# Optimization experiments

Hardware: AMD Instinct MI355X
Metric: run time of the kernel (lower is better)

The kernel has to match this reference:

```python
import jax, jax.numpy as jnp
import numpy as np
import math

T_LEN, BATCH, DIN, DH, DT = 512, 64, 512, 512, 128


def _u(key, shape, std):
    return jax.random.uniform(key, shape, jnp.float32, -std, std)


def setup_inputs() -> dict:
    key = jax.random.key(0)
    ks = jax.random.split(key, 32)
    std = 1.0 / math.sqrt(DH)
    inp = {
        'x': jax.random.normal(ks[0], (T_LEN, BATCH, DIN), jnp.float32),
        'topic': jax.random.normal(ks[1], (BATCH, DT), jnp.float32),
        'mask': jnp.ones((T_LEN, BATCH), jnp.float32),
        # weights stored as [in, out] (transpose of nn.Linear), uniform(-std, std)
        'W_x2zr': _u(ks[2], (DIN, 2 * DH), std),
        'W_tp2zr_x': _u(ks[3], (DT, 2 * DH), std),
        'W_xtp2z': _u(ks[4], (DH, DH), std),
        'b_xtp2z': _u(ks[5], (DH,), std),
        'W_xtp2r': _u(ks[6], (DH, DH), std),
        'b_xtp2r': _u(ks[7], (DH,), std),
        'W_h2zr': _u(ks[8], (DH, 2 * DH), std),
        'W_tp2zr_h': _u(ks[9], (DT, 2 * DH), std),
        'W_htp2z': _u(ks[10], (DH, DH), std),
        'W_htp2r': _u(ks[11], (DH, DH), std),
        'W_x2h': _u(ks[12], (DIN, DH), std),
        'W_tp2h_x': _u(ks[13], (DT, DH), std),
        'W_xtp2h': _u(ks[14], (DH, DH), std),
        'b_xtp2h': _u(ks[15], (DH,), std),
        'W_h2h': _u(ks[16], (DH, DH), std),
        'W_tp2h_h': _u(ks[17], (DT, DH), std),
        'W_htp2h': _u(ks[18], (DH, DH), std),
    }
    return inp


def _tpgru_forward(x, topic, mask,
                   W_x2zr, W_tp2zr_x, W_xtp2z, b_xtp2z, W_xtp2r, b_xtp2r,
                   W_h2zr, W_tp2zr_h, W_htp2z, W_htp2r,
                   W_x2h, W_tp2h_x, W_xtp2h, b_xtp2h,
                   W_h2h, W_tp2h_h, W_htp2h):
    # Precompute all time-parallel (input-side) projections outside the scan.
    ZR_x = x @ W_x2zr                          # [T,B,2H]
    tp_zr_x = topic @ W_tp2zr_x                # [B,2H]
    tp_zr_h = topic @ W_tp2zr_h                # [B,2H]
    Z_xtp, R_xtp = jnp.split(ZR_x * tp_zr_x[None], 2, axis=-1)
    ZR_xtp = jnp.concatenate([Z_xtp @ W_xtp2z + b_xtp2z,
                              R_xtp @ W_xtp2r + b_xtp2r], axis=-1)  # [T,B,2H]
    tp_h_x = topic @ W_tp2h_x                  # [B,H]
    tp_h_h = topic @ W_tp2h_h                  # [B,H]
    H_xtp = ((x @ W_x2h) * tp_h_x[None]) @ W_xtp2h + b_xtp2h        # [T,B,H]

    def step(h_, inputs):
        zr_xtp, h_xtp, m = inputs              # [B,2H], [B,H], [B]
        zr_htp = (h_ @ W_h2zr) * tp_zr_h
        z_htp, r_htp = jnp.split(zr_htp, 2, axis=-1)
        pre_zr = jax.nn.sigmoid(zr_xtp + jnp.concatenate(
            [z_htp @ W_htp2z, r_htp @ W_htp2r], axis=-1))
        z, r = jnp.split(pre_zr, 2, axis=-1)
        h = jnp.tanh(h_xtp + r * (((h_ @ W_h2h) * tp_h_h) @ W_htp2h))
        h = (1.0 - z) * h + z * h_
        m = m[:, None]
        h = m * h + (1.0 - m) * h_
        return h, h

    h0 = jnp.zeros((x.shape[1], W_h2h.shape[0]), x.dtype)
    hT, output = jax.lax.scan(step, h0, (ZR_xtp, H_xtp, mask))
    return output, hT[None]                    # [T,B,H], [1,B,H]


def reference(x, topic, mask,
              W_x2zr, W_tp2zr_x, W_xtp2z, b_xtp2z, W_xtp2r, b_xtp2r,
              W_h2zr, W_tp2zr_h, W_htp2z, W_htp2r,
              W_x2h, W_tp2h_x, W_xtp2h, b_xtp2h,
              W_h2h, W_tp2h_h, W_htp2h):
    return _tpgru_forward(x, topic, mask,
                          W_x2zr, W_tp2zr_x, W_xtp2z, b_xtp2z, W_xtp2r, b_xtp2r,
                          W_h2zr, W_tp2zr_h, W_htp2z, W_htp2r,
                          W_x2h, W_tp2h_x, W_xtp2h, b_xtp2h,
                          W_h2h, W_tp2h_h, W_htp2h)
```

## Files before the change

### kernel.cpp

```cpp
#include <hip/hip_runtime.h>
#include <stdint.h>
#include <stddef.h>


#define T_LEN 512
#define BATCH 64
#define DIN   512
#define DH    512
#define DT    128

typedef __attribute__((ext_vector_type(8))) short short8;
typedef __attribute__((ext_vector_type(4))) float f32x4;

static __device__ __forceinline__ float bf2f(unsigned short u) {
  unsigned v = ((unsigned)u) << 16;
  return __builtin_bit_cast(float, v);
}
static __device__ __forceinline__ unsigned short f2bf(float f) {
  unsigned v = __builtin_bit_cast(unsigned, f);
  unsigned r = (v + 0x7fffu + ((v >> 16) & 1u)) >> 16;
  return (unsigned short)r;
}
static __device__ __forceinline__ float sigmoid_f(float x) {
  return 1.f / (1.f + __expf(-x));
}
static __device__ __forceinline__ float tanh_f(float x) {
  float e = __expf(-2.f * fabsf(x));
  float t = (1.f - e) / (1.f + e);
  return copysignf(t, x);
}

static __device__ __forceinline__ void bstore_u16(unsigned short* p, unsigned short v) {
  __hip_atomic_store(p, v, __ATOMIC_RELAXED, __HIP_MEMORY_SCOPE_AGENT);
}

template<bool F32>
static __device__ __forceinline__ void load8(const void* p, size_t off, unsigned short* d) {
  if (F32) {
    const float4* q = (const float4*)((const float*)p + off);
    float4 a = q[0], b = q[1];
    d[0] = f2bf(a.x); d[1] = f2bf(a.y); d[2] = f2bf(a.z); d[3] = f2bf(a.w);
    d[4] = f2bf(b.x); d[5] = f2bf(b.y); d[6] = f2bf(b.z); d[7] = f2bf(b.w);
  } else {
    *(uint4*)d = *(const uint4*)((const unsigned short*)p + off);
  }
}

__global__ __launch_bounds__(256) void k_topic(
    const float* __restrict__ topic,
    const float* __restrict__ Wzx,
    const float* __restrict__ Wzh,
    const float* __restrict__ Whx,
    const float* __restrict__ Whh,
    float* __restrict__ tzx, float* __restrict__ tzh,
    float* __restrict__ thx, float* __restrict__ thh)
{
  const int b = blockIdx.x;
  __shared__ float tp[DT];
  if (threadIdx.x < DT) tp[threadIdx.x] = topic[b * DT + threadIdx.x];
  __syncthreads();
  for (int c = threadIdx.x; c < 3072; c += 256) {
    const float* wp; float* op; int ld, cc;
    if (c < 1024)      { wp = Wzx; ld = 1024; cc = c;        op = &tzx[b*1024 + cc]; }
    else if (c < 2048) { wp = Wzh; ld = 1024; cc = c - 1024; op = &tzh[b*1024 + cc]; }
    else if (c < 2560) { wp = Whx; ld = 512;  cc = c - 2048; op = &thx[b*512  + cc]; }
    else               { wp = Whh; ld = 512;  cc = c - 2560; op = &thh[b*512  + cc]; }
    float acc = 0.f;
    #pragma unroll 4
    for (int k = 0; k < DT; ++k) acc += tp[k] * wp[(size_t)k * ld + cc];
    *op = acc;
  }
}

template<int EPI, bool AF32, bool BF32>
__global__ __launch_bounds__(256) void gemm64(
    const void* __restrict__ A, int lda,
    const void* __restrict__ B1, int ldb1,
    const float* __restrict__ rs1, int ldrs1,
    const float* __restrict__ bias,
    unsigned short* __restrict__ C, int ldc, int K)
{
  __shared__ unsigned short As[64][48];
  __shared__ unsigned short Bs[64][48];
  const int tid = threadIdx.x;
  const int n0 = blockIdx.x * 64;
  const int m0 = blockIdx.y * 64;
  const int wv = tid >> 6, lane = tid & 63;
  const int lh = lane & 15, q8 = (lane >> 4) * 8;
  const int arow = tid >> 2, acol = (tid & 3) * 8;
  const int brow = tid >> 3, bcol = (tid & 7) * 8;
  f32x4 acc[4] = {{0,0,0,0},{0,0,0,0},{0,0,0,0},{0,0,0,0}};

  for (int k0 = 0; k0 < K; k0 += 32) {
    unsigned short av[8], bv[8];
    load8<AF32>(A, (size_t)(m0 + arow) * lda + (k0 + acol), av);
    load8<BF32>(B1, (size_t)(k0 + brow) * ldb1 + (n0 + bcol), bv);
    __syncthreads();
    *(uint4*)(&As[arow][acol]) = *(const uint4*)av;
    #pragma unroll
    for (int i = 0; i < 8; ++i) Bs[bcol + i][brow] = bv[i];
    __syncthreads();
    short8 af = *(const short8*)(&As[wv * 16 + lh][q8]);
    #pragma unroll
    for (int nt = 0; nt < 4; ++nt) {
      short8 bf = *(const short8*)(&Bs[nt * 16 + lh][q8]);
      acc[nt] = __builtin_amdgcn_mfma_f32_16x16x32_bf16(af, bf, acc[nt], 0, 0, 0);
    }
  }

  #pragma unroll
  for (int nt = 0; nt < 4; ++nt) {
    #pragma unroll
    for (int r = 0; r < 4; ++r) {
      int row = m0 + wv * 16 + (lane >> 4) * 4 + r;
      int colc = nt * 16 + lh;
      float v = acc[nt][r];
      if (EPI == 0) v *= rs1[(size_t)(row & 63) * ldrs1 + (n0 + colc)];
      else          v += bias[n0 + colc];
      C[(size_t)row * ldc + (n0 + colc)] = f2bf(v);
    }
  }
}

__global__ __launch_bounds__(256) void k_comb(
    const float* __restrict__ W1, int ld1, int off1,
    const float* __restrict__ W2,
    const float* __restrict__ S, int ldS, int offS,
    unsigned short* __restrict__ Cout)
{
  __shared__ unsigned short As[64][48];
  __shared__ unsigned short Bs[64][48];
  const int tid = threadIdx.x;
  const int n0 = blockIdx.x * 64;
  const int m0 = blockIdx.y * 64;
  const int b  = blockIdx.z;
  const int wv = tid >> 6, lane = tid & 63;
  const int lh = lane & 15, q8 = (lane >> 4) * 8;
  const int arow = tid >> 2, acol = (tid & 3) * 8;
  const int brow = tid >> 3, bcol = (tid & 7) * 8;
  const float* sv = S + (size_t)b * ldS + offS;
  f32x4 acc[4] = {{0,0,0,0},{0,0,0,0},{0,0,0,0},{0,0,0,0}};

  for (int k0 = 0; k0 < 512; k0 += 32) {
    unsigned short av[8], bv[8];
    {
      const float* p = W1 + (size_t)(m0 + arow) * ld1 + off1 + k0 + acol;
      float4 a = ((const float4*)p)[0], c2 = ((const float4*)p)[1];
      av[0]=f2bf(a.x); av[1]=f2bf(a.y); av[2]=f2bf(a.z); av[3]=f2bf(a.w);
      av[4]=f2bf(c2.x); av[5]=f2bf(c2.y); av[6]=f2bf(c2.z); av[7]=f2bf(c2.w);
    }
    {
      float sk = sv[k0 + brow];
      const float* p = W2 + (size_t)(k0 + brow) * 512 + n0 + bcol;
      float4 a = ((const float4*)p)[0], c2 = ((const float4*)p)[1];
      bv[0]=f2bf(a.x*sk); bv[1]=f2bf(a.y*sk); bv[2]=f2bf(a.z*sk); bv[3]=f2bf(a.w*sk);
      bv[4]=f2bf(c2.x*sk); bv[5]=f2bf(c2.y*sk); bv[6]=f2bf(c2.z*sk); bv[7]=f2bf(c2.w*sk);
    }
    __syncthreads();
    *(uint4*)(&As[arow][acol]) = *(const uint4*)av;
    #pragma unroll
    for (int i = 0; i < 8; ++i) Bs[bcol + i][brow] = bv[i];
    __syncthreads();
    short8 af = *(const short8*)(&As[wv * 16 + lh][q8]);
    #pragma unroll
    for (int nt = 0; nt < 4; ++nt) {
      short8 bf = *(const short8*)(&Bs[nt * 16 + lh][q8]);
      acc[nt] = __builtin_amdgcn_mfma_f32_16x16x32_bf16(af, bf, acc[nt], 0, 0, 0);
    }
  }

  #pragma unroll
  for (int nt = 0; nt < 4; ++nt) {
    #pragma unroll
    for (int r = 0; r < 4; ++r) {
      int row = m0 + wv * 16 + (lane >> 4) * 4 + r;
      int col = n0 + nt * 16 + lh;
      Cout[(size_t)b * 262144 + (size_t)row * 512 + col] = f2bf(acc[nt][r]);
    }
  }
}

static __device__ __forceinline__ void gbar(int* bar, int target) {
  asm volatile("s_waitcnt vmcnt(0)" ::: "memory");
  __syncthreads();
  if (threadIdx.x == 0) {
    __hip_atomic_fetch_add(bar, 1, __ATOMIC_RELAXED, __HIP_MEMORY_SCOPE_AGENT);
    while (__hip_atomic_load(bar, __ATOMIC_RELAXED, __HIP_MEMORY_SCOPE_AGENT) < target)
      __builtin_amdgcn_s_sleep(1);
  }
  __syncthreads();
}

static __device__ __forceinline__ void accum8(float* a, float hk, uint4 v) {
  unsigned u0 = v.x, u1 = v.y, u2 = v.z, u3 = v.w;
  a[0] += hk * __builtin_bit_cast(float, u0 << 16);
  a[1] += hk * __builtin_bit_cast(float, u0 & 0xffff0000u);
  a[2] += hk * __builtin_bit_cast(float, u1 << 16);
  a[3] += hk * __builtin_bit_cast(float, u1 & 0xffff0000u);
  a[4] += hk * __builtin_bit_cast(float, u2 << 16);
  a[5] += hk * __builtin_bit_cast(float, u2 & 0xffff0000u);
  a[6] += hk * __builtin_bit_cast(float, u3 << 16);
  a[7] += hk * __builtin_bit_cast(float, u3 & 0xffff0000u);
}

__global__ __launch_bounds__(512) void k_scan2(
    const unsigned short* __restrict__ Az,
    const unsigned short* __restrict__ Ar,
    const unsigned short* __restrict__ Ah,
    const unsigned short* __restrict__ ZRx,
    const unsigned short* __restrict__ Hx,
    const float* __restrict__ mask,
    unsigned short* hbuf,
    float* out, int* bar)
{
  const int g = blockIdx.x;
  const int b = g >> 3;
  const int o = g & 7;
  const int c0 = o * 64;
  const int t = threadIdx.x;
  const int chunk = t & 7;
  const int ph = t >> 3;
  __shared__ float hs[512];
  __shared__ float part[64][8][25];
  int* mybar = bar + b * 32;

  const size_t mbase = (size_t)b * 262144 + (size_t)ph * 512 + c0 + chunk * 8;
  const unsigned short* pz0 = Az + mbase;
  const unsigned short* pr0 = Ar + mbase;
  const unsigned short* pv0 = Ah + mbase;

  float hold = 0.f;
  int ep = 0;

  for (int tm = 0; tm < T_LEN; ++tm) {
    const int cur = tm & 1;
    const size_t itb = (size_t)tm * BATCH + b;
    float g_zx = 0.f, g_rx = 0.f, g_hx = 0.f, g_m = 0.f;
    if (t < 64) {
      int gc = c0 + t;
      g_zx = bf2f(ZRx[itb * 1024 + gc]);
      g_rx = bf2f(ZRx[itb * 1024 + 512 + gc]);
      g_hx = bf2f(Hx[itb * 512 + gc]);
      g_m  = mask[itb];
    }
    if (t < 256) {
      unsigned v = __hip_atomic_load(
          (const unsigned*)(hbuf + ((size_t)cur * 64 + b) * 512) + t,
          __ATOMIC_RELAXED, __HIP_MEMORY_SCOPE_AGENT);
      hs[2 * t]     = bf2f((unsigned short)(v & 0xffffu));
      hs[2 * t + 1] = bf2f((unsigned short)(v >> 16));
    }
    __syncthreads();

    float az[8] = {0,0,0,0,0,0,0,0};
    float ar[8] = {0,0,0,0,0,0,0,0};
    float av[8] = {0,0,0,0,0,0,0,0};
    #pragma unroll
    for (int j = 0; j < 8; ++j) {
      float hk = hs[ph + 64 * j];
      uint4 vz = *(const uint4*)(pz0 + (size_t)j * 64 * 512);
      uint4 vr = *(const uint4*)(pr0 + (size_t)j * 64 * 512);
      uint4 vv = *(const uint4*)(pv0 + (size_t)j * 64 * 512);
      accum8(az, hk, vz);
      accum8(ar, hk, vr);
      accum8(av, hk, vv);
    }
    #pragma unroll
    for (int e = 0; e < 8; ++e) {
      part[ph][chunk][e]      = az[e];
      part[ph][chunk][8 + e]  = ar[e];
      part[ph][chunk][16 + e] = av[e];
    }
    __syncthreads();

    if (t < 64) {
      int gc = c0 + t;
      int ch = t >> 3, e = t & 7;
      float sz = 0.f, sr = 0.f, sh = 0.f;
      #pragma unroll 8
      for (int p = 0; p < 64; ++p) {
        sz += part[p][ch][e];
        sr += part[p][ch][8 + e];
        sh += part[p][ch][16 + e];
      }
      float z  = sigmoid_f(sz + g_zx);
      float r  = sigmoid_f(sr + g_rx);
      float hv = tanh_f(g_hx + r * sh);
      float hnew = (1.f - z) * hv + z * hold;
      hnew = g_m * hnew + (1.f - g_m) * hold;
      hold = hnew;
      out[itb * 512 + gc] = hnew;
      if (tm == T_LEN - 1)
        out[(size_t)T_LEN * BATCH * 512 + (size_t)b * 512 + gc] = hnew;
      bstore_u16(hbuf + ((size_t)(cur ^ 1) * 64 + b) * 512 + gc, f2bf(hnew));
    }
    ++ep;
    gbar(mybar, 8 * ep);
  }
}

extern "C" void kernel_launch(void* const* d_in, const int* in_sizes, int n_in,
                              void* d_out, int out_size, void* d_ws, size_t ws_size,
                              hipStream_t stream) {
  (void)in_sizes; (void)n_in; (void)out_size; (void)ws_size;
  const float* x        = (const float*)d_in[0];
  const float* topic    = (const float*)d_in[1];
  const float* mask     = (const float*)d_in[2];
  const float* W_x2zr   = (const float*)d_in[3];
  const float* W_tp2zrx = (const float*)d_in[4];
  const float* W_xtp2z  = (const float*)d_in[5];
  const float* b_xtp2z  = (const float*)d_in[6];
  const float* W_xtp2r  = (const float*)d_in[7];
  const float* b_xtp2r  = (const float*)d_in[8];
  const float* W_h2zr   = (const float*)d_in[9];
  const float* W_tp2zrh = (const float*)d_in[10];
  const float* W_htp2z  = (const float*)d_in[11];
  const float* W_htp2r  = (const float*)d_in[12];
  const float* W_x2h    = (const float*)d_in[13];
  const float* W_tp2hx  = (const float*)d_in[14];
  const float* W_xtp2h  = (const float*)d_in[15];
  const float* b_xtp2h  = (const float*)d_in[16];
  const float* W_h2h    = (const float*)d_in[17];
  const float* W_tp2hh  = (const float*)d_in[18];
  const float* W_htp2h  = (const float*)d_in[19];
  float* out = (float*)d_out;

  char* w = (char*)d_ws;
  int*            bar  = (int*)w;            w += 8192;
  unsigned short* hbuf = (unsigned short*)w; w += (size_t)2 * BATCH * 512 * 2;
  float* tzx = (float*)w;           w += (size_t)BATCH * 1024 * 4;
  float* tzh = (float*)w;           w += (size_t)BATCH * 1024 * 4;
  float* thx = (float*)w;           w += (size_t)BATCH * 512 * 4;
  float* thh = (float*)w;           w += (size_t)BATCH * 512 * 4;
  unsigned short* ZRxtp = (unsigned short*)w; w += (size_t)T_LEN * BATCH * 1024 * 2;
  unsigned short* Hxtp  = (unsigned short*)w; w += (size_t)T_LEN * BATCH * 512 * 2;
  unsigned short* SCR   = (unsigned short*)w; w += (size_t)T_LEN * BATCH * 1024 * 2;
  unsigned short* AhM   = (unsigned short*)w; w += (size_t)BATCH * 512 * 512 * 2;
  unsigned short* ZRs = SCR;
  unsigned short* Xhs = SCR;
  unsigned short* AzM = SCR;
  unsigned short* ArM = SCR + (size_t)BATCH * 512 * 512;

  const int M = T_LEN * BATCH;

  hipMemsetAsync(bar, 0, 8192 + (size_t)2 * BATCH * 512 * 2, stream);

  k_topic<<<BATCH, 256, 0, stream>>>(topic, W_tp2zrx, W_tp2zrh, W_tp2hx, W_tp2hh,
                                     tzx, tzh, thx, thh);
  gemm64<0, true, true><<<dim3(1024/64, M/64), 256, 0, stream>>>(
      x, DIN, W_x2zr, 1024, tzx, 1024, nullptr, ZRs, 1024, DIN);
  gemm64<1, false, true><<<dim3(512/64, M/64), 256, 0, stream>>>(
      ZRs, 1024, W_xtp2z, 512, nullptr, 0, b_xtp2z, ZRxtp, 1024, 512);
  gemm64<1, false, true><<<dim3(512/64, M/64), 256, 0, stream>>>(
      ZRs + 512, 1024, W_xtp2r, 512, nullptr, 0, b_xtp2r, ZRxtp + 512, 1024, 512);
  gemm64<0, true, true><<<dim3(512/64, M/64), 256, 0, stream>>>(
      x, DIN, W_x2h, 512, thx, 512, nullptr, Xhs, 512, DIN);
  gemm64<1, false, true><<<dim3(512/64, M/64), 256, 0, stream>>>(
      Xhs, 512, W_xtp2h, 512, nullptr, 0, b_xtp2h, Hxtp, 512, 512);

  k_comb<<<dim3(8, 8, 64), 256, 0, stream>>>(W_h2zr, 1024,   0, W_htp2z, tzh, 1024,   0, AzM);
  k_comb<<<dim3(8, 8, 64), 256, 0, stream>>>(W_h2zr, 1024, 512, W_htp2r, tzh, 1024, 512, ArM);
  k_comb<<<dim3(8, 8, 64), 256, 0, stream>>>(W_h2h,   512,   0, W_htp2h, thh,  512,   0, AhM);

  k_scan2<<<512, 512, 0, stream>>>(AzM, ArM, AhM, ZRxtp, Hxtp, mask,
                                   hbuf, out, bar);
}
```

Before: 4.975 ms.

## Replace per-step atomic barrier with per-slice flag publishing in GRU scan

Drops the counter barrier (fetch-add plus spin) that every block hit each timestep. Each block now writes its packed bf16 hidden slice next to a per-slice step tag in a double-buffered publish area, and consumers spin on the eight tags before reading h. The final reduction is also split across 192 threads instead of 64. Each step should wait less, but correctness now rests on relaxed atomics plus the vmcnt wait ordering the data stores before the tag store.

```diff
diff --git a/kernel.cpp b/kernel.cpp
--- a/kernel.cpp
+++ b/kernel.cpp
@@ -28,10 +28,6 @@
   float e = __expf(-2.f * fabsf(x));
   float t = (1.f - e) / (1.f + e);
   return copysignf(t, x);
-}
-
-static __device__ __forceinline__ void bstore_u16(unsigned short* p, unsigned short v) {
-  __hip_atomic_store(p, v, __ATOMIC_RELAXED, __HIP_MEMORY_SCOPE_AGENT);
 }
 
 template<bool F32>
@@ -180,17 +176,6 @@
   }
 }
 
-static __device__ __forceinline__ void gbar(int* bar, int target) {
-  asm volatile("s_waitcnt vmcnt(0)" ::: "memory");
-  __syncthreads();
-  if (threadIdx.x == 0) {
-    __hip_atomic_fetch_add(bar, 1, __ATOMIC_RELAXED, __HIP_MEMORY_SCOPE_AGENT);
-    while (__hip_atomic_load(bar, __ATOMIC_RELAXED, __HIP_MEMORY_SCOPE_AGENT) < target)
-      __builtin_amdgcn_s_sleep(1);
-  }
-  __syncthreads();
-}
-
 static __device__ __forceinline__ void accum8(float* a, float hk, uint4 v) {
   unsigned u0 = v.x, u1 = v.y, u2 = v.z, u3 = v.w;
   a[0] += hk * __builtin_bit_cast(float, u0 << 16);
@@ -203,38 +188,41 @@
   a[7] += hk * __builtin_bit_cast(float, u3 & 0xffff0000u);
 }
 
-__global__ __launch_bounds__(512) void k_scan2(
+__global__ __launch_bounds__(512) void k_scan3(
     const unsigned short* __restrict__ Az,
     const unsigned short* __restrict__ Ar,
     const unsigned short* __restrict__ Ah,
     const unsigned short* __restrict__ ZRx,
     const unsigned short* __restrict__ Hx,
     const float* __restrict__ mask,
-    unsigned short* hbuf,
-    float* out, int* bar)
+    unsigned* __restrict__ pub,
+    float* out)
 {
   const int g = blockIdx.x;
   const int b = g >> 3;
-  const int o = g & 7;
-  const int c0 = o * 64;
+  const int w = g & 7;
+  const int c0 = w * 64;
   const int t = threadIdx.x;
   const int chunk = t & 7;
   const int ph = t >> 3;
   __shared__ float hs[512];
   __shared__ float part[64][8][25];
-  int* mybar = bar + b * 32;
+  __shared__ float red[192];
 
   const size_t mbase = (size_t)b * 262144 + (size_t)ph * 512 + c0 + chunk * 8;
   const unsigned short* pz0 = Az + mbase;
   const unsigned short* pr0 = Ar + mbase;
   const unsigned short* pv0 = Ah + mbase;
 
+  unsigned* pubB0 = pub + (size_t)b * 512;
+  unsigned* pubB1 = pub + (size_t)(64 + b) * 512;
+
   float hold = 0.f;
-  int ep = 0;
-
   for (int tm = 0; tm < T_LEN; ++tm) {
-    const int cur = tm & 1;
+    unsigned* pubC = (tm & 1) ? pubB1 : pubB0;
+    unsigned* pubP = (tm & 1) ? pubB0 : pubB1;
     const size_t itb = (size_t)tm * BATCH + b;
+
     float g_zx = 0.f, g_rx = 0.f, g_hx = 0.f, g_m = 0.f;
     if (t < 64) {
       int gc = c0 + t;
@@ -243,12 +231,18 @@
       g_hx = bf2f(Hx[itb * 512 + gc]);
       g_m  = mask[itb];
     }
+    if (t < 8) {
+      const unsigned* tagp = pubC + t * 64 + 32;
+      while ((int)__hip_atomic_load(tagp, __ATOMIC_RELAXED, __HIP_MEMORY_SCOPE_AGENT) < tm)
+        ;
+    }
+    __syncthreads();
     if (t < 256) {
-      unsigned v = __hip_atomic_load(
-          (const unsigned*)(hbuf + ((size_t)cur * 64 + b) * 512) + t,
-          __ATOMIC_RELAXED, __HIP_MEMORY_SCOPE_AGENT);
-      hs[2 * t]     = bf2f((unsigned short)(v & 0xffffu));
-      hs[2 * t + 1] = bf2f((unsigned short)(v >> 16));
+      unsigned v = __hip_atomic_load(pubC + (t >> 5) * 64 + (t & 31),
+                                     __ATOMIC_RELAXED, __HIP_MEMORY_SCOPE_AGENT);
+      int col = (t >> 5) * 64 + (t & 31) * 2;
+      hs[col]     = bf2f((unsigned short)(v & 0xffffu));
+      hs[col + 1] = bf2f((unsigned short)(v >> 16));
     }
     __syncthreads();
 
@@ -273,29 +267,39 @@
     }
     __syncthreads();
 
+    if (t < 192) {
+      int c = t & 63;
+      int ch = c >> 3;
+      int e  = (t >> 6) * 8 + (c & 7);
+      float s = 0.f;
+      #pragma unroll 16
+      for (int p = 0; p < 64; ++p) s += part[p][ch][e];
+      red[t] = s;
+    }
+    __syncthreads();
+
     if (t < 64) {
-      int gc = c0 + t;
-      int ch = t >> 3, e = t & 7;
-      float sz = 0.f, sr = 0.f, sh = 0.f;
-      #pragma unroll 8
-      for (int p = 0; p < 64; ++p) {
-        sz += part[p][ch][e];
-        sr += part[p][ch][8 + e];
-        sh += part[p][ch][16 + e];
-      }
-      float z  = sigmoid_f(sz + g_zx);
-      float r  = sigmoid_f(sr + g_rx);
-      float hv = tanh_f(g_hx + r * sh);
+      float z  = sigmoid_f(red[t] + g_zx);
+      float r  = sigmoid_f(red[64 + t] + g_rx);
+      float hv = tanh_f(g_hx + r * red[128 + t]);
       float hnew = (1.f - z) * hv + z * hold;
       hnew = g_m * hnew + (1.f - g_m) * hold;
       hold = hnew;
+      int gc = c0 + t;
       out[itb * 512 + gc] = hnew;
       if (tm == T_LEN - 1)
         out[(size_t)T_LEN * BATCH * 512 + (size_t)b * 512 + gc] = hnew;
-      bstore_u16(hbuf + ((size_t)(cur ^ 1) * 64 + b) * 512 + gc, f2bf(hnew));
-    }
-    ++ep;
-    gbar(mybar, 8 * ep);
+      int hb = (int)f2bf(hnew);
+      unsigned lo = (unsigned)__shfl(hb, 2 * t);
+      unsigned hi = (unsigned)__shfl(hb, 2 * t + 1);
+      if (t < 32)
+        __hip_atomic_store(pubP + w * 64 + t, lo | (hi << 16),
+                           __ATOMIC_RELAXED, __HIP_MEMORY_SCOPE_AGENT);
+      asm volatile("s_waitcnt vmcnt(0)" ::: "memory");
+      if (t == 0)
+        __hip_atomic_store(pubP + w * 64 + 32, (unsigned)(tm + 1),
+                           __ATOMIC_RELAXED, __HIP_MEMORY_SCOPE_AGENT);
+    }
   }
 }
 
@@ -326,8 +330,7 @@
   float* out = (float*)d_out;
 
   char* w = (char*)d_ws;
-  int*            bar  = (int*)w;            w += 8192;
-  unsigned short* hbuf = (unsigned short*)w; w += (size_t)2 * BATCH * 512 * 2;
+  unsigned* pub = (unsigned*)w;      w += (size_t)2 * 64 * 8 * 64 * 4;
   float* tzx = (float*)w;           w += (size_t)BATCH * 1024 * 4;
   float* tzh = (float*)w;           w += (size_t)BATCH * 1024 * 4;
   float* thx = (float*)w;           w += (size_t)BATCH * 512 * 4;
@@ -343,7 +346,7 @@
 
   const int M = T_LEN * BATCH;
 
-  hipMemsetAsync(bar, 0, 8192 + (size_t)2 * BATCH * 512 * 2, stream);
+  hipMemsetAsync(pub, 0, (size_t)2 * 64 * 8 * 64 * 4, stream);
 
   k_topic<<<BATCH, 256, 0, stream>>>(topic, W_tp2zrx, W_tp2zrh, W_tp2hx, W_tp2hh,
                                      tzx, tzh, thx, thh);
@@ -362,6 +365,6 @@
   k_comb<<<dim3(8, 8, 64), 256, 0, stream>>>(W_h2zr, 1024, 512, W_htp2r, tzh, 1024, 512, ArM);
   k_comb<<<dim3(8, 8, 64), 256, 0, stream>>>(W_h2h,   512,   0, W_htp2h, thh,  512,   0, AhM);
 
-  k_scan2<<<512, 512, 0, stream>>>(AzM, ArM, AhM, ZRxtp, Hxtp, mask,
-                                   hbuf, out, bar);
-}
+  k_scan3<<<512, 512, 0, stream>>>(AzM, ArM, AhM, ZRxtp, Hxtp, mask,
+                                   pub, out);
+}
```

Measured after the change: 4.185 ms. -15.9%, faster.
